# Performance work log

Hardware: AMD Instinct MI355X
Metric: run time of the kernel (lower is better)

## Reference

```python
import jax, jax.numpy as jnp
import numpy as np

NUM_SPECIES = 4
NUM_PAIRS = NUM_SPECIES * (NUM_SPECIES + 1) // 2  # 10
RCR = 5.2   # radial cutoff (Angstrom)
RCA = 3.5   # angular cutoff
ETA_R = 16.0
SHF_R = jnp.asarray(0.9 + (RCR - 0.9) / 16.0 * np.arange(16), dtype=jnp.float32)  # 16 radial shifts
ETA_A = 8.0
ZETA = 32.0
SHF_A = jnp.asarray(0.9 + (RCA - 0.9) / 4.0 * np.arange(4), dtype=jnp.float32)    # 4 angular radial shifts
SHF_Z = jnp.asarray(np.pi / 16.0 * (2 * np.arange(8) + 1), dtype=jnp.float32)      # 8 angle shifts
RADIAL_SUB, ANGULAR_SUB = 16, 32

def _triu_index(ns):
    # species-pair (s1,s2) -> packed upper-triangular pair index, symmetric
    i, j = np.triu_indices(ns)
    t = np.zeros((ns, ns), dtype=np.int32)
    t[i, j] = np.arange(len(i))
    t[j, i] = t[i, j]
    return jnp.asarray(t)

TRIU = _triu_index(NUM_SPECIES)

def cosine_cutoff(d, rc):
    return jnp.where(d <= rc, 0.5 * jnp.cos(jnp.pi * d / rc) + 0.5, 0.0)

def compute_aev(species, coordinates):
    N, A = species.shape
    eye = jnp.eye(A, dtype=bool)
    # v_ij = r_j - r_i  (N,A,A,3)
    diff = coordinates[:, None, :, :] - coordinates[:, :, None, :]
    d2 = jnp.sum(diff * diff, axis=-1)
    dist = jnp.sqrt(jnp.where(eye, 1.0, d2))  # safe diagonal for sqrt grad

    # ---- radial AEV: sum_j 0.25*exp(-eta*(d-shf)^2)*fc(d), binned by species[j]
    pm = (~eye) & (dist <= RCR)
    fc_r = jnp.where(pm, cosine_cutoff(dist, RCR), 0.0)
    rt = 0.25 * jnp.exp(-ETA_R * (dist[..., None] - SHF_R) ** 2) * fc_r[..., None]  # (N,A,A,16)
    oh = jax.nn.one_hot(species, NUM_SPECIES, dtype=rt.dtype)                        # (N,A,S)
    radial = jnp.einsum('nijr,njs->nisr', rt, oh).reshape(N, A, NUM_SPECIES * RADIAL_SUB)

    # ---- angular AEV: triplets (center i, sides j<k) within angular cutoff
    am = (~eye) & (dist <= RCA)
    fc_a = jnp.where(am, cosine_cutoff(dist, RCA), 0.0)
    u = diff / dist[..., None]
    cosang = 0.95 * jnp.einsum('nijd,nikd->nijk', u, u)  # torchani's 0.95 acos guard
    ang = jnp.arccos(cosang)
    jk = jnp.triu(jnp.ones((A, A), dtype=bool), k=1)     # count each unordered pair once
    mask3 = am[:, :, :, None] & am[:, :, None, :] & jk[None, None]
    fprod = jnp.where(mask3, fc_a[:, :, :, None] * fc_a[:, :, None, :], 0.0)
    f1 = ((1.0 + jnp.cos(ang[..., None] - SHF_Z)) * 0.5) ** ZETA                    # (N,A,A,A,8)
    davg = 0.5 * (dist[:, :, :, None] + dist[:, :, None, :])
    f2 = jnp.exp(-ETA_A * (davg[..., None] - SHF_A) ** 2)                            # (N,A,A,A,4)
    terms = (2.0 * fprod)[..., None, None] * f2[..., :, None] * f1[..., None, :]     # (N,A,A,A,4,8)
    # species-pair bin of the two side atoms
    poh = jax.nn.one_hot(TRIU[species[:, :, None], species[:, None, :]], NUM_PAIRS, dtype=rt.dtype)  # (N,A,A,P)
    angular = jnp.einsum('nijkt,njkp->nipt', terms.reshape(N, A, A, A, ANGULAR_SUB), poh)
    angular = angular.reshape(N, A, NUM_PAIRS * ANGULAR_SUB)

    return jnp.concatenate([radial, angular], axis=-1)  # (N, A, 384)

def setup_inputs() -> dict:
    key = jax.random.key(0)
    k1, k2 = jax.random.split(key)
    species = jax.random.randint(k1, (8, 64), 0, NUM_SPECIES, dtype=jnp.int32)
    coordinates = jax.random.uniform(k2, (8, 64, 3), dtype=jnp.float32) * 10.0
    return {"species": species, "coordinates": coordinates}

def reference(species, coordinates):
    # SpeciesAEV returns (species, aev); species passes through unchanged, so return aev
    return compute_aev(species, coordinates)
```

## Files before the change

kernel.cpp:

```cpp
#include <hip/hip_runtime.h>
#include <hip/hip_bf16.h>
#include <math.h>

#define A_ATOMS 64
#define AEVDIM  384

__global__ __launch_bounds__(64) void aev_kernel(
    const int*   __restrict__ species,
    const float* __restrict__ coords,
    float*       __restrict__ out)
{
    constexpr float PI  = 3.14159265358979323846f;
    constexpr float RCR = 5.2f;
    constexpr float RCA = 3.5f;

    const int bid  = blockIdx.x;
    const int n    = bid >> 6;
    const int i    = bid & 63;
    const int lane = threadIdx.x;

    __shared__ float sh_aev[AEVDIM];
    __shared__ float s_cx[64], s_cy[64], s_cz[64];
    __shared__ float s_ux[64], s_uy[64], s_uz[64], s_d[64], s_fc[64];
    __shared__ int   s_nspec[64];

    for (int f = lane; f < AEVDIM; f += 64) sh_aev[f] = 0.0f;

    const float* cb = coords + (size_t)n * (A_ATOMS * 3);
    const float xj = cb[lane * 3 + 0];
    const float yj = cb[lane * 3 + 1];
    const float zj = cb[lane * 3 + 2];
    const int   sj = species[n * A_ATOMS + lane];
    s_cx[lane] = xj; s_cy[lane] = yj; s_cz[lane] = zj;
    __syncthreads();

    const float xi = s_cx[i], yi = s_cy[i], zi = s_cz[i];
    const float dx = xj - xi, dy = yj - yi, dz = zj - zi;
    const float d  = sqrtf(dx * dx + dy * dy + dz * dz);
    const bool  notself = (lane != i);

    if (notself && d <= RCR) {
        const float fc = 0.5f * cosf(PI * (d * (1.0f / RCR))) + 0.5f;
        const float q  = 0.25f * fc;
        float* dst = &sh_aev[sj * 16];
        #pragma unroll
        for (int r = 0; r < 16; ++r) {
            const float shf = 0.9f + 0.26875f * (float)r;
            const float t   = d - shf;
            atomicAdd(&dst[r], q * expf(-16.0f * t * t));
        }
    }

    const bool act = notself && (d <= RCA);
    const unsigned long long bm = __ballot(act);
    const int M = __popcll(bm);
    if (act) {
        const int pos = __popcll(bm & ((1ull << lane) - 1ull));
        const float inv = 1.0f / d;
        s_ux[pos] = dx * inv; s_uy[pos] = dy * inv; s_uz[pos] = dz * inv;
        s_d[pos]  = d;
        s_fc[pos] = 0.5f * cosf(PI * (d * (1.0f / RCA))) + 0.5f;
        s_nspec[pos] = sj;
    }
    __syncthreads();

    const float CZ[8] = { 0.980785280f,  0.831469612f,  0.555570233f,  0.195090322f,
                         -0.195090322f, -0.555570233f, -0.831469612f, -0.980785280f };
    const float SZ[8] = { 0.195090322f,  0.555570233f,  0.831469612f,  0.980785280f,
                          0.980785280f,  0.831469612f,  0.555570233f,  0.195090322f };

    const int nP = (M * (M - 1)) >> 1;
    for (int p = lane; p < nP; p += 64) {
        int a = 0, rem = p;
        while (rem >= (M - 1 - a)) { rem -= (M - 1 - a); ++a; }
        const int b = a + 1 + rem;

        const float fp2  = 2.0f * s_fc[a] * s_fc[b];
        const float dot  = s_ux[a] * s_ux[b] + s_uy[a] * s_uy[b] + s_uz[a] * s_uz[b];
        const float ca   = 0.95f * dot;
        const float sa   = sqrtf(fmaxf(0.0f, 1.0f - ca * ca));
        const float davg = 0.5f * (s_d[a] + s_d[b]);

        const int s1 = s_nspec[a], s2 = s_nspec[b];
        const int lo = (s1 < s2) ? s1 : s2;
        const int hi = (s1 < s2) ? s2 : s1;
        const int pb = ((lo * (9 - lo)) >> 1) + (hi - lo);
        float* dst = &sh_aev[64 + pb * 32];

        #pragma unroll
        for (int aa = 0; aa < 4; ++aa) {
            const float shfa = 0.9f + 0.65f * (float)aa;
            const float t    = davg - shfa;
            const float base = fp2 * expf(-8.0f * t * t);
            #pragma unroll
            for (int z = 0; z < 8; ++z) {
                const float c  = ca * CZ[z] + sa * SZ[z];
                float f1 = 0.5f * (1.0f + c);
                f1 = f1 * f1; f1 = f1 * f1; f1 = f1 * f1; f1 = f1 * f1; f1 = f1 * f1;
                atomicAdd(&dst[aa * 8 + z], base * f1);
            }
        }
    }
    __syncthreads();

    float* o = out + (size_t)bid * AEVDIM;
    for (int f = lane; f < AEVDIM; f += 64) o[f] = sh_aev[f];
}

extern "C" void kernel_launch(void* const* d_in, const int* in_sizes, int n_in,
                              void* d_out, int out_size, void* d_ws, size_t ws_size,
                              hipStream_t stream) {
    const int*   species = (const int*)d_in[0];
    const float* coords  = (const float*)d_in[1];
    float*       out     = (float*)d_out;
    const int N = in_sizes[0] / A_ATOMS;
    aev_kernel<<<N * A_ATOMS, 64, 0, stream>>>(species, coords, out);
}
```

Before: 16.23 us.

## Use four waves per atom block and split radial/angular shifts across waves

Each block now runs 256 threads (four wavefronts) instead of one. The four radial shift groups and the four angular radial shifts are spread across the waves, so each thread does a quarter of the exp and atomic work per pair. cosf and expf are also swapped for the fast __cosf and __expf intrinsics. The cost is four times the threads per block, redundant distance and ballot computation in every wave, and slightly lower transcendental accuracy.

New measurement: 15.20 us. 1.07x faster.

```diff
diff --git a/kernel.cpp b/kernel.cpp
--- a/kernel.cpp
+++ b/kernel.cpp
@@ -5,7 +5,7 @@
 #define A_ATOMS 64
 #define AEVDIM  384
 
-__global__ __launch_bounds__(64) void aev_kernel(
+__global__ __launch_bounds__(256) void aev_kernel(
     const int*   __restrict__ species,
     const float* __restrict__ coords,
     float*       __restrict__ out)
@@ -17,49 +17,52 @@
     const int bid  = blockIdx.x;
     const int n    = bid >> 6;
     const int i    = bid & 63;
-    const int lane = threadIdx.x;
+    const int t    = threadIdx.x;
+    const int lane = t & 63;
+    const int wid  = t >> 6;
 
     __shared__ float sh_aev[AEVDIM];
     __shared__ float s_cx[64], s_cy[64], s_cz[64];
+    __shared__ int   s_spec[64];
     __shared__ float s_ux[64], s_uy[64], s_uz[64], s_d[64], s_fc[64];
     __shared__ int   s_nspec[64];
 
-    for (int f = lane; f < AEVDIM; f += 64) sh_aev[f] = 0.0f;
-
-    const float* cb = coords + (size_t)n * (A_ATOMS * 3);
-    const float xj = cb[lane * 3 + 0];
-    const float yj = cb[lane * 3 + 1];
-    const float zj = cb[lane * 3 + 2];
-    const int   sj = species[n * A_ATOMS + lane];
-    s_cx[lane] = xj; s_cy[lane] = yj; s_cz[lane] = zj;
+    for (int f = t; f < AEVDIM; f += 256) sh_aev[f] = 0.0f;
+    if (t < 64) {
+        const float* cb = coords + (size_t)n * (A_ATOMS * 3) + t * 3;
+        s_cx[t] = cb[0]; s_cy[t] = cb[1]; s_cz[t] = cb[2];
+        s_spec[t] = species[n * A_ATOMS + t];
+    }
     __syncthreads();
 
     const float xi = s_cx[i], yi = s_cy[i], zi = s_cz[i];
-    const float dx = xj - xi, dy = yj - yi, dz = zj - zi;
+    const float dx = s_cx[lane] - xi, dy = s_cy[lane] - yi, dz = s_cz[lane] - zi;
     const float d  = sqrtf(dx * dx + dy * dy + dz * dz);
     const bool  notself = (lane != i);
+    const int   sj = s_spec[lane];
 
     if (notself && d <= RCR) {
-        const float fc = 0.5f * cosf(PI * (d * (1.0f / RCR))) + 0.5f;
+        const float fc = 0.5f * __cosf(PI * (d * (1.0f / RCR))) + 0.5f;
         const float q  = 0.25f * fc;
         float* dst = &sh_aev[sj * 16];
         #pragma unroll
-        for (int r = 0; r < 16; ++r) {
+        for (int rr = 0; rr < 4; ++rr) {
+            const int   r   = wid * 4 + rr;
             const float shf = 0.9f + 0.26875f * (float)r;
-            const float t   = d - shf;
-            atomicAdd(&dst[r], q * expf(-16.0f * t * t));
+            const float tt  = d - shf;
+            atomicAdd(&dst[r], q * __expf(-16.0f * tt * tt));
         }
     }
 
     const bool act = notself && (d <= RCA);
     const unsigned long long bm = __ballot(act);
     const int M = __popcll(bm);
-    if (act) {
+    if (wid == 0 && act) {
         const int pos = __popcll(bm & ((1ull << lane) - 1ull));
         const float inv = 1.0f / d;
         s_ux[pos] = dx * inv; s_uy[pos] = dy * inv; s_uz[pos] = dz * inv;
         s_d[pos]  = d;
-        s_fc[pos] = 0.5f * cosf(PI * (d * (1.0f / RCA))) + 0.5f;
+        s_fc[pos] = 0.5f * __cosf(PI * (d * (1.0f / RCA))) + 0.5f;
         s_nspec[pos] = sj;
     }
     __syncthreads();
@@ -69,8 +72,10 @@
     const float SZ[8] = { 0.195090322f,  0.555570233f,  0.831469612f,  0.980785280f,
                           0.980785280f,  0.831469612f,  0.555570233f,  0.195090322f };
 
-    const int nP = (M * (M - 1)) >> 1;
-    for (int p = lane; p < nP; p += 64) {
+    const int nTask = ((M * (M - 1)) >> 1) << 2;
+    for (int task = t; task < nTask; task += 256) {
+        const int p  = task >> 2;
+        const int aa = task & 3;
         int a = 0, rem = p;
         while (rem >= (M - 1 - a)) { rem -= (M - 1 - a); ++a; }
         const int b = a + 1 + rem;
@@ -85,26 +90,24 @@
         const int lo = (s1 < s2) ? s1 : s2;
         const int hi = (s1 < s2) ? s2 : s1;
         const int pb = ((lo * (9 - lo)) >> 1) + (hi - lo);
-        float* dst = &sh_aev[64 + pb * 32];
+
+        const float shfa = 0.9f + 0.65f * (float)aa;
+        const float tt   = davg - shfa;
+        const float base = fp2 * __expf(-8.0f * tt * tt);
+        float* dst = &sh_aev[64 + pb * 32 + aa * 8];
 
         #pragma unroll
-        for (int aa = 0; aa < 4; ++aa) {
-            const float shfa = 0.9f + 0.65f * (float)aa;
-            const float t    = davg - shfa;
-            const float base = fp2 * expf(-8.0f * t * t);
-            #pragma unroll
-            for (int z = 0; z < 8; ++z) {
-                const float c  = ca * CZ[z] + sa * SZ[z];
-                float f1 = 0.5f * (1.0f + c);
-                f1 = f1 * f1; f1 = f1 * f1; f1 = f1 * f1; f1 = f1 * f1; f1 = f1 * f1;
-                atomicAdd(&dst[aa * 8 + z], base * f1);
-            }
+        for (int z = 0; z < 8; ++z) {
+            const float c  = ca * CZ[z] + sa * SZ[z];
+            float f1 = 0.5f * (1.0f + c);
+            f1 = f1 * f1; f1 = f1 * f1; f1 = f1 * f1; f1 = f1 * f1; f1 = f1 * f1;
+            atomicAdd(&dst[z], base * f1);
         }
     }
     __syncthreads();
 
     float* o = out + (size_t)bid * AEVDIM;
-    for (int f = lane; f < AEVDIM; f += 64) o[f] = sh_aev[f];
+    for (int f = t; f < AEVDIM; f += 256) o[f] = sh_aev[f];
 }
 
 extern "C" void kernel_launch(void* const* d_in, const int* in_sizes, int n_in,
@@ -114,5 +117,5 @@
     const float* coords  = (const float*)d_in[1];
     float*       out     = (float*)d_out;
     const int N = in_sizes[0] / A_ATOMS;
-    aev_kernel<<<N * A_ATOMS, 64, 0, stream>>>(species, coords, out);
+    aev_kernel<<<N * A_ATOMS, 256, 0, stream>>>(species, coords, out);
 }
```
